# Kernel optimization log

Hardware: AMD Instinct MI355X
Metric: run time of the kernel (lower is better)

## Reference

```python
import math
import jax, jax.numpy as jnp
import numpy as np

DIM = 1536
HEADS = 8
DK = 64
DV = 192
NRPF = 192  # num_rel_pos_features, divisible by 6
SEQ = 1536
BATCH = 4
SCALE = DK ** -0.5


def get_positional_embed(n, feature_size):
    # distances in [-(n-1), n-1], length 2n-1
    dist = jnp.arange(-n + 1, n).astype(jnp.float32)
    adist = jnp.abs(dist)[:, None]  # [2n-1, 1]
    f = feature_size // 6  # 3 feature fns, each doubled by sign channel
    # exponential half-life features
    max_range = math.log(n) / math.log(2.0)
    half_life = 2.0 ** jnp.linspace(3.0, max_range, f)[None, :]
    emb_exp = jnp.exp(-math.log(2.0) / half_life * adist)
    # central mask features
    center_widths = (2.0 ** jnp.arange(1, f + 1).astype(jnp.float32) - 1.0)[None, :]
    emb_cm = (center_widths > adist).astype(jnp.float32)
    # gamma pdf features
    stddev = n / (2.0 * f)
    start_mean = n / float(f)
    mean = jnp.linspace(start_mean, float(n), f)[None, :]
    conc = (mean / stddev) ** 2
    rate = mean / stddev ** 2
    log_unnorm = (conc - 1.0) * jnp.log(jnp.maximum(adist, 1e-20)) - rate * adist
    log_norm = jax.scipy.special.gammaln(conc) - conc * jnp.log(rate)
    prob = jnp.exp(log_unnorm - log_norm) + 1e-8
    emb_g = prob / jnp.max(prob, axis=-1, keepdims=True)
    emb = jnp.concatenate([emb_exp, emb_cm, emb_g], axis=-1)  # [2n-1, feat/2]
    return jnp.concatenate([emb, jnp.sign(dist)[:, None] * emb], axis=-1)  # [2n-1, feat]


def relative_shift(x):
    # x: [b, h, n, 2n-1] -> [b, h, n, n] via the Transformer-XL shift trick
    b, h, t1, t2 = x.shape
    x = jnp.concatenate([jnp.zeros_like(x[..., :1]), x], axis=-1)  # [b,h,t1,t2+1]
    x = x.reshape(b, h, t2 + 1, t1)[:, :, 1:, :].reshape(b, h, t1, t2)
    return x[..., : (t2 + 2) // 2]


def layer_norm(x, g, b, eps=1e-5):
    mu = jnp.mean(x, axis=-1, keepdims=True)
    var = jnp.var(x, axis=-1, keepdims=True)
    return (x - mu) * jax.lax.rsqrt(var + eps) * g + b


def setup_inputs() -> dict:
    key = jax.random.key(0)
    ks = jax.random.split(key, 16)
    d, h, dk, dv = DIM, HEADS, DK, DV
    inp = {
        "x": jax.random.normal(ks[0], (BATCH, SEQ, d), dtype=jnp.float32),
        "ln1_g": jnp.ones((d,), jnp.float32),
        "ln1_b": jnp.zeros((d,), jnp.float32),
        "Wq": jax.random.normal(ks[1], (d, h * dk), jnp.float32) / math.sqrt(d),
        "Wk": jax.random.normal(ks[2], (d, h * dk), jnp.float32) / math.sqrt(d),
        "Wv": jax.random.normal(ks[3], (d, h * dv), jnp.float32) / math.sqrt(d),
        "Wo": jax.random.normal(ks[4], (h * dv, d), jnp.float32) / math.sqrt(h * dv),
        "bo": jnp.zeros((d,), jnp.float32),
        "Wrk": jax.random.normal(ks[5], (NRPF, h * dk), jnp.float32) / math.sqrt(NRPF),
        "rel_content_bias": jax.random.normal(ks[6], (1, h, 1, dk), jnp.float32),
        "rel_pos_bias": jax.random.normal(ks[7], (1, h, 1, dk), jnp.float32),
        "ln2_g": jnp.ones((d,), jnp.float32),
        "ln2_b": jnp.zeros((d,), jnp.float32),
        "W1": jax.random.normal(ks[8], (d, 2 * d), jnp.float32) / math.sqrt(d),
        "b1": jnp.zeros((2 * d,), jnp.float32),
        "W2": jax.random.normal(ks[9], (2 * d, d), jnp.float32) / math.sqrt(2 * d),
        "b2": jnp.zeros((d,), jnp.float32),
    }
    return inp


def _attention(x, Wq, Wk, Wv, Wo, bo, Wrk, rel_content_bias, rel_pos_bias):
    b, n, _ = x.shape
    h, dk, dv = HEADS, DK, DV
    q = (x @ Wq).reshape(b, n, h, dk).transpose(0, 2, 1, 3) * SCALE  # [b,h,n,dk]
    k = (x @ Wk).reshape(b, n, h, dk).transpose(0, 2, 1, 3)
    v = (x @ Wv).reshape(b, n, h, dv).transpose(0, 2, 1, 3)
    content_logits = jnp.einsum('bhid,bhjd->bhij', q + rel_content_bias, k)
    positions = get_positional_embed(n, NRPF)  # [2n-1, NRPF]
    rel_k = (positions @ Wrk).reshape(2 * n - 1, h, dk).transpose(1, 0, 2)  # [h,2n-1,dk]
    rel_logits = jnp.einsum('bhid,hjd->bhij', q + rel_pos_bias, rel_k)
    rel_logits = relative_shift(rel_logits)  # [b,h,n,n]
    attn = jax.nn.softmax(content_logits + rel_logits, axis=-1)
    out = jnp.einsum('bhij,bhjd->bhid', attn, v)
    out = out.transpose(0, 2, 1, 3).reshape(b, n, h * dv)
    return out @ Wo + bo


def reference(x, ln1_g, ln1_b, Wq, Wk, Wv, Wo, bo, Wrk, rel_content_bias,
              rel_pos_bias, ln2_g, ln2_b, W1, b1, W2, b2):
    # pre-LN attention with residual
    x = x + _attention(layer_norm(x, ln1_g, ln1_b), Wq, Wk, Wv, Wo, bo, Wrk,
                       rel_content_bias, rel_pos_bias)
    # MLP block (carries its own LayerNorm and residual)
    y = layer_norm(x, ln2_g, ln2_b)
    y = jax.nn.relu(y @ W1 + b1)
    y = y @ W2 + b2
    return y + x
```

## Files before the change

### kernel.cpp

```cpp
#include <hip/hip_runtime.h>
#include <hip/hip_bf16.h>
#include <math.h>

#define SEQN 1536
#define NH 8
#define MROWS 6144
#define NDIST 3071

typedef __attribute__((ext_vector_type(8))) _Float16 f16x8;
typedef __attribute__((ext_vector_type(4))) _Float16 f16x4;
typedef __attribute__((ext_vector_type(4))) float f32x4;

#define MFMAH(a, b, c) __builtin_amdgcn_mfma_f32_16x16x32_f16(a, b, c, 0, 0, 0)

__device__ __forceinline__ void gl_lds16(const void* g, void* l) {
  __builtin_amdgcn_global_load_lds(
      (const __attribute__((address_space(1))) void*)g,
      (__attribute__((address_space(3))) void*)l, 16, 0, 0);
}

__global__ __launch_bounds__(64) void pos_embed_kernel(float* __restrict__ pos) {
  int row = blockIdx.x;
  int j = threadIdx.x;
  if (j >= 32) return;
  float dist = (float)(row - (SEQN - 1));
  float adist = fabsf(dist);
  float sgn = (dist > 0.f) ? 1.f : (dist < 0.f ? -1.f : 0.f);

  const float max_range = 10.58496250072116f;
  float hl = exp2f(3.0f + ((max_range - 3.0f) / 31.0f) * (float)j);
  float e_exp = expf(-0.6931471805599453f / hl * adist);

  float cw = exp2f((float)(j + 1)) - 1.0f;
  float e_cm = (cw > adist) ? 1.0f : 0.0f;

  float mean = 48.0f * (float)(j + 1);
  float tt = mean / 24.0f;
  float conc = tt * tt;
  float rate = mean / 576.0f;
  float log_unnorm = (conc - 1.0f) * logf(fmaxf(adist, 1e-20f)) - rate * adist;
  float log_norm = lgammaf(conc) - conc * logf(rate);
  float prob = expf(log_unnorm - log_norm) + 1e-8f;
  float mx = prob;
  #pragma unroll
  for (int off = 16; off >= 1; off >>= 1)
    mx = fmaxf(mx, __shfl_xor(mx, off, 32));
  float e_g = prob / mx;

  float* o = pos + (size_t)row * 192;
  o[j] = e_exp;        o[32 + j] = e_cm;        o[64 + j] = e_g;
  o[96 + j] = sgn * e_exp; o[128 + j] = sgn * e_cm; o[160 + j] = sgn * e_g;
}

__global__ __launch_bounds__(512) void relk_kernel(
    const float* __restrict__ pos, const float* __restrict__ Wrk,
    const float* __restrict__ pb, _Float16* __restrict__ rk, float* __restrict__ PR) {
  __shared__ float prow[16][192];
  const int d0 = blockIdx.x * 16;
  const int t = threadIdx.x;
  #pragma unroll
  for (int p = 0; p < 6; ++p) {
    int idx = t + p * 512;
    int r = idx / 192, c = idx - r * 192;
    prow[r][c] = pos[(size_t)(d0 + r) * 192 + c];
  }
  __syncthreads();
  float acc[16];
  #pragma unroll
  for (int r = 0; r < 16; ++r) acc[r] = 0.f;
  #pragma unroll 4
  for (int kk = 0; kk < 192; ++kk) {
    float wv = Wrk[(size_t)kk * 512 + t];
    #pragma unroll
    for (int r = 0; r < 16; ++r) acc[r] = fmaf(prow[r][kk], wv, acc[r]);
  }
  #pragma unroll
  for (int r = 0; r < 16; ++r)
    rk[(size_t)(d0 + r) * 512 + t] = (_Float16)acc[r];
  float pbv = pb[t];
  #pragma unroll
  for (int r = 0; r < 16; ++r) {
    float pv = pbv * acc[r];
    #pragma unroll
    for (int off = 32; off >= 1; off >>= 1) pv += __shfl_xor(pv, off);
    if ((t & 63) == 0 && (d0 + r) < NDIST)
      PR[(size_t)(t >> 6) * NDIST + d0 + r] = pv;
  }
}

__global__ __launch_bounds__(256) void ck_kernel(
    const _Float16* __restrict__ Kp, const float* __restrict__ cb,
    float* __restrict__ CK) {
  const int gid = blockIdx.x * 4 + (threadIdx.x >> 6);
  const int lane = threadIdx.x & 63;
  const int row = gid >> 3;
  const int h = gid & 7;
  float kv = (float)Kp[(size_t)row * 512 + h * 64 + lane];
  float pv = cb[h * 64 + lane] * kv;
  #pragma unroll
  for (int off = 32; off >= 1; off >>= 1) pv += __shfl_xor(pv, off);
  if (lane == 0) CK[(size_t)row * 8 + h] = pv;
}

__global__ __launch_bounds__(256) void ln_kernel(
    const float* __restrict__ x, const float* __restrict__ g,
    const float* __restrict__ bta, _Float16* __restrict__ oh) {
  const int row = blockIdx.x;
  const int t = threadIdx.x;
  __shared__ float red[4];
  __shared__ float bc[2];
  const float4* xr = (const float4*)(x + (size_t)row * 1536);
  float4 v0 = xr[t];
  float4 v1 = make_float4(0.f, 0.f, 0.f, 0.f);
  if (t < 128) v1 = xr[256 + t];
  float s = v0.x + v0.y + v0.z + v0.w;
  if (t < 128) s += v1.x + v1.y + v1.z + v1.w;
  #pragma unroll
  for (int off = 32; off >= 1; off >>= 1) s += __shfl_xor(s, off);
  if ((t & 63) == 0) red[t >> 6] = s;
  __syncthreads();
  if (t == 0) bc[0] = (red[0] + red[1] + red[2] + red[3]) * (1.f / 1536.f);
  __syncthreads();
  const float mu = bc[0];
  float d, s2 = 0.f;
  d = v0.x - mu; s2 += d * d; d = v0.y - mu; s2 += d * d;
  d = v0.z - mu; s2 += d * d; d = v0.w - mu; s2 += d * d;
  if (t < 128) {
    d = v1.x - mu; s2 += d * d; d = v1.y - mu; s2 += d * d;
    d = v1.z - mu; s2 += d * d; d = v1.w - mu; s2 += d * d;
  }
  #pragma unroll
  for (int off = 32; off >= 1; off >>= 1) s2 += __shfl_xor(s2, off);
  if ((t & 63) == 0) red[t >> 6] = s2;
  __syncthreads();
  if (t == 0) bc[1] = (red[0] + red[1] + red[2] + red[3]) * (1.f / 1536.f);
  __syncthreads();
  const float inv = rsqrtf(bc[1] + 1e-5f);
  const float4* g4 = (const float4*)g;
  const float4* b4 = (const float4*)bta;
  float4 gg = g4[t], bb = b4[t];
  f16x4 hv;
  hv[0] = (_Float16)((v0.x - mu) * inv * gg.x + bb.x);
  hv[1] = (_Float16)((v0.y - mu) * inv * gg.y + bb.y);
  hv[2] = (_Float16)((v0.z - mu) * inv * gg.z + bb.z);
  hv[3] = (_Float16)((v0.w - mu) * inv * gg.w + bb.w);
  *(f16x4*)(oh + (size_t)row * 1536 + t * 4) = hv;
  if (t < 128) {
    gg = g4[256 + t]; bb = b4[256 + t];
    hv[0] = (_Float16)((v1.x - mu) * inv * gg.x + bb.x);
    hv[1] = (_Float16)((v1.y - mu) * inv * gg.y + bb.y);
    hv[2] = (_Float16)((v1.z - mu) * inv * gg.z + bb.z);
    hv[3] = (_Float16)((v1.w - mu) * inv * gg.w + bb.w);
    *(f16x4*)(oh + (size_t)row * 1536 + 1024 + t * 4) = hv;
  }
}

__global__ __launch_bounds__(256) void convw_kernel(
    const float* __restrict__ W, _Float16* __restrict__ Th,
    int N, int K, int KD, int roff, float scale) {
  __shared__ float tile[32][33];
  const int n0 = blockIdx.x * 32, k0 = blockIdx.y * 32;
  const int t = threadIdx.x;
  const int cr = t >> 5;
  const int cc = t & 31;
  #pragma unroll
  for (int p = 0; p < 4; ++p) {
    int r = cr + p * 8;
    tile[r][cc] = W[(size_t)(k0 + r) * N + n0 + cc];
  }
  __syncthreads();
  #pragma unroll
  for (int p = 0; p < 4; ++p) {
    int r = cr + p * 8;
    float v = tile[cc][r] * scale;
    Th[(size_t)(roff + n0 + r) * KD + k0 + cc] = (_Float16)v;
  }
}

template <int EPI, int BNJ>
__global__ __launch_bounds__(256, 4) void mgemm_kernel(
    const _Float16* __restrict__ A, const _Float16* __restrict__ B,
    float* __restrict__ C, _Float16* __restrict__ Ch,
    _Float16* __restrict__ Kp, _Float16* __restrict__ Vt,
    const float* __restrict__ bias, const float* __restrict__ res,
    int M, int N, int K) {
  constexpr int BN = BNJ * 32;
  __shared__ _Float16 sm[8192 + BN * 64];
  const int t = threadIdx.x;
  const int lane = t & 63;
  const int w = t >> 6;
  const int wm = w >> 1, wn = w & 1;
  const int slab = (M >> 7) >> 3;
  const int xcd = blockIdx.x & 7;
  const int r = blockIdx.x >> 3;
  const int yt = xcd * slab + (r % slab);
  const int xt = r / slab;
  const int m0 = yt * 128, n0 = xt * BN;

  f32x4 acc[4][BNJ];
  #pragma unroll
  for (int i = 0; i < 4; ++i)
    #pragma unroll
    for (int j = 0; j < BNJ; ++j) acc[i][j] = (f32x4){0.f, 0.f, 0.f, 0.f};

  const int srow = t >> 3;
  const int ssl = t & 7;
  const int ss = ssl ^ (srow & 7);
  const int lr = lane & 15;
  const int g = lane >> 4;
  const int kb = lr & 7;

  for (int k0 = 0; k0 < K; k0 += 64) {
    #pragma unroll
    for (int p = 0; p < 4; ++p) {
      int row = srow + p * 32;
      gl_lds16(A + (size_t)(m0 + row) * K + k0 + ss * 8, &sm[row * 64 + ssl * 8]);
    }
    #pragma unroll
    for (int p = 0; p < BN / 32; ++p) {
      int row = srow + p * 32;
      gl_lds16(B + (size_t)(n0 + row) * K + k0 + ss * 8,
               &sm[8192 + row * 64 + ssl * 8]);
    }
    __syncthreads();
    #pragma unroll
    for (int h2 = 0; h2 < 2; ++h2) {
      const int ksl = ((h2 * 4 + g) ^ kb) * 8;
      f16x8 a[4], b[BNJ];
      #pragma unroll
      for (int i = 0; i < 4; ++i)
        a[i] = *(const f16x8*)(&sm[(wm * 64 + i * 16 + lr) * 64 + ksl]);
      #pragma unroll
      for (int j = 0; j < BNJ; ++j)
        b[j] = *(const f16x8*)(&sm[8192 + (wn * BNJ * 16 + j * 16 + lr) * 64 + ksl]);
      #pragma unroll
      for (int i = 0; i < 4; ++i)
        #pragma unroll
        for (int j = 0; j < BNJ; ++j)
          acc[i][j] = MFMAH(a[i], b[j], acc[i][j]);
    }
    __syncthreads();
  }

  const int lq = lane >> 4;
  #pragma unroll
  for (int i = 0; i < 4; ++i) {
    #pragma unroll
    for (int j = 0; j < BNJ; ++j) {
      const int c0 = n0 + wn * BNJ * 16 + j * 16;
      const int col = c0 + lr;
      const int rbase = m0 + wm * 64 + i * 16 + lq * 4;
      if (EPI == 3) {
        #pragma unroll
        for (int q = 0; q < 4; ++q) {
          size_t o = (size_t)(rbase + q) * N + col;
          C[o] = acc[i][j][q] + bias[col] + res[o];
        }
      } else if (EPI == 2) {
        #pragma unroll
        for (int q = 0; q < 4; ++q) {
          size_t o = (size_t)(rbase + q) * N + col;
          Ch[o] = (_Float16)fmaxf(acc[i][j][q] + bias[col], 0.f);
        }
      } else {
        if (c0 < 512) {
          #pragma unroll
          for (int q = 0; q < 4; ++q)
            Ch[(size_t)(rbase + q) * 512 + col] = (_Float16)acc[i][j][q];
        } else if (c0 < 1024) {
          #pragma unroll
          for (int q = 0; q < 4; ++q)
            Kp[(size_t)(rbase + q) * 512 + (col - 512)] = (_Float16)acc[i][j][q];
        } else {
          int dv = col - 1024;
          int hd = dv / 192;
          int dvh = dv - hd * 192;
          int bb = rbase / 1536;
          int nloc = rbase - bb * 1536;
          f16x4 pk;
          pk[0] = (_Float16)acc[i][j][0];
          pk[1] = (_Float16)acc[i][j][1];
          pk[2] = (_Float16)acc[i][j][2];
          pk[3] = (_Float16)acc[i][j][3];
          *(f16x4*)(Vt + (((size_t)bb * 8 + hd) * 192 + dvh) * 1536 + nloc) = pk;
        }
      }
    }
  }
}

__global__ __launch_bounds__(256, 3) void attn_kernel(
    const _Float16* __restrict__ Qp, const _Float16* __restrict__ Kp,
    const _Float16* __restrict__ Vt, const _Float16* __restrict__ rk,
    const float* __restrict__ PR, const float* __restrict__ CK,
    _Float16* __restrict__ ao) {
  __shared__ _Float16 lds[26752];
  const int id = blockIdx.x;
  const int xcd = id & 7, s = id >> 3;
  const int bh = xcd * 4 + s / 24;
  const int it = s % 24;
  const int b = bh >> 3, h = bh & 7;
  const int t = threadIdx.x;
  const int w = t >> 6;
  const int lane = t & 63;
  const int c15 = lane & 15, g = lane >> 4;
  const int swz = c15 & 7;
  const int vsz = (c15 >> 1) & 3;
  const int qrow0 = it * 64 + w * 16;
  const int rrow0 = 48 - w * 16;
  const int R0 = 1472 - it * 64;

  const int lr = lane >> 3, sl = lane & 7;
  const int ss = sl ^ lr;
  const int ss2 = (lane & 3) ^ ((lane >> 3) & 3);

  f16x8 qh0, qh1;
  {
    size_t qo = ((size_t)(b * SEQN + qrow0 + c15)) * 512 + h * 64 + g * 8;
    qh0 = *(const f16x8*)(Qp + qo);
    qh1 = *(const f16x8*)(Qp + qo + 32);
  }
  const float* PRrow = PR + (size_t)h * NDIST;
  const float* CKb2 = CK + (size_t)b * SEQN * 8 + h;

  f32x4 acc[12];
  #pragma unroll
  for (int d = 0; d < 12; ++d) acc[d] = (f32x4){0.f, 0.f, 0.f, 0.f};
  float mrun[4], lrun[4];
  #pragma unroll
  for (int q = 0; q < 4; ++q) { mrun[q] = -1e30f; lrun[q] = 0.f; }

  #define STAGE_KV(J0, KB, VB)                                                   \
    do {                                                                         \
      size_t gk = ((size_t)(b * SEQN + (J0) + w * 8 + lr)) * 512 + h * 64 + ss * 8; \
      gl_lds16(Kp + gk, &lds[(KB) + w * 512]);                                   \
      _Pragma("unroll") for (int p = 0; p < 3; ++p) {                            \
        int rv = w * 48 + p * 16 + (lane >> 2);                                  \
        size_t gv = (((size_t)(b * 8 + h)) * 192 + rv) * SEQN + (J0) + ss2 * 8;  \
        gl_lds16(Vt + gv, &lds[(VB) + (w * 48 + p * 16) * 32]);                  \
      }                                                                          \
    } while (0)

  #define STAGE_R_PRO()                                                          \
    do {                                                                         \
      _Pragma("unroll") for (int p = 0; p < 4; ++p) {                            \
        int rr = w * 32 + p * 8 + lr;                                            \
        size_t gr = ((size_t)(R0 + rr)) * 512 + h * 64 + ss * 8;                 \
        gl_lds16(rk + gr, &lds[16384 + (w * 32 + p * 8) * 64]);                  \
      }                                                                          \
    } while (0)

  #define STAGE_R_INC(REL0)                                                      \
    do {                                                                         \
      int rr = (REL0) + w * 8 + lr;                                              \
      size_t gr = ((size_t)(R0 + rr)) * 512 + h * 64 + ss * 8;                   \
      gl_lds16(rk + gr, &lds[16384 + ((((REL0) + w * 8) & 127)) * 64]);          \
    } while (0)

  #define COMP_T(DST, ETOFF)                                                     \
    do {                                                                         \
      int relrow = (cc32 + rrow0 + (ETOFF) + c15) & 127;                         \
      f16x8 r0_ = *(const f16x8*)(&lds[16384 + relrow * 64 + (g ^ swz) * 8]);    \
      f16x8 r1_ = *(const f16x8*)(&lds[16384 + relrow * 64 + ((4 + g) ^ swz) * 8]); \
      f32x4 tt_ = (f32x4){0.f, 0.f, 0.f, 0.f};                                   \
      tt_ = MFMAH(qh0, r0_, tt_);                                                \
      tt_ = MFMAH(qh1, r1_, tt_);                                                \
      float prv_ = PRrow[dbase + (ETOFF) + c15];                                 \
      _Pragma("unroll") for (int q = 0; q < 4; ++q) tt_[q] += prv_;              \
      DST = tt_;                                                                 \
    } while (0)

  STAGE_KV(0, 0, 4096);
  STAGE_R_PRO();

  f32x4 T0, T1, T2;

  for (int c = 0; c < 48; ++c) {
    const int j0 = c * 32;
    const int cc32 = c * 32;
    const int cur = c & 1;
    const int KB = cur * 2048;
    const int VB = 4096 + cur * 6144;
    __syncthreads();

    if (c < 47) STAGE_KV(j0 + 32, (cur ^ 1) * 2048, 4096 + (cur ^ 1) * 6144);

    const int dbase = 1520 + j0 - qrow0;
    __builtin_amdgcn_s_setprio(1);
    if (c == 0) {
      COMP_T(T0, 0);
    } else {
      T0 = T2;
    }
    COMP_T(T1, 16);
    COMP_T(T2, 32);
    f32x4 S[2];
    #pragma unroll
    for (int st = 0; st < 2; ++st) {
      int rowK = st * 16 + c15;
      f16x8 kh0 = *(const f16x8*)(&lds[KB + rowK * 64 + (g ^ swz) * 8]);
      f16x8 kh1 = *(const f16x8*)(&lds[KB + rowK * 64 + ((4 + g) ^ swz) * 8]);
      f32x4 ssv = (f32x4){0.f, 0.f, 0.f, 0.f};
      ssv = MFMAH(qh0, kh0, ssv);
      ssv = MFMAH(qh1, kh1, ssv);
      S[st] = ssv;
    }
    __builtin_amdgcn_s_setprio(0);
    float ck0 = CKb2[(size_t)(j0 + c15) * 8];
    float ck1 = CKb2[(size_t)(j0 + 16 + c15) * 8];
    #pragma unroll
    for (int q = 0; q < 4; ++q) {
      int eoff = c15 + 15 - 4 * g - q;
      int src = (lane & 48) | (eoff & 15);
      float t0v = __shfl(T0[q], src);
      float t1v = __shfl(T1[q], src);
      float t2v = __shfl(T2[q], src);
      bool lo = eoff < 16;
      S[0][q] += ck0 + (lo ? t0v : t1v);
      S[1][q] += ck1 + (lo ? t1v : t2v);
    }
    int need = 0;
    #pragma unroll
    for (int st = 0; st < 2; ++st)
      #pragma unroll
      for (int q = 0; q < 4; ++q) need |= (S[st][q] > mrun[q] + 8.0f) ? 1 : 0;
    if (__any(need)) {
      float mx[4];
      #pragma unroll
      for (int q = 0; q < 4; ++q) mx[q] = fmaxf(S[0][q], S[1][q]);
      #pragma unroll
      for (int off = 8; off >= 1; off >>= 1)
        #pragma unroll
        for (int q = 0; q < 4; ++q) mx[q] = fmaxf(mx[q], __shfl_xor(mx[q], off));
      #pragma unroll
      for (int q = 0; q < 4; ++q) {
        float mn = fmaxf(mrun[q], mx[q]);
        float al = __expf(mrun[q] - mn);
        mrun[q] = mn;
        lrun[q] *= al;
        #pragma unroll
        for (int d = 0; d < 12; ++d) acc[d][q] *= al;
      }
    }
    float pv16[2][4], sum[4];
    #pragma unroll
    for (int q = 0; q < 4; ++q) sum[q] = 0.f;
    #pragma unroll
    for (int st = 0; st < 2; ++st)
      #pragma unroll
      for (int q = 0; q < 4; ++q) {
        float p = __expf(S[st][q] - mrun[q]);
        sum[q] += p;
        pv16[st][q] = p;
      }
    #pragma unroll
    for (int off = 8; off >= 1; off >>= 1)
      #pragma unroll
      for (int q = 0; q < 4; ++q) sum[q] += __shfl_xor(sum[q], off);
    #pragma unroll
    for (int q = 0; q < 4; ++q) lrun[q] += sum[q];

    #pragma unroll
    for (int st = 0; st < 2; ++st)
      #pragma unroll
      for (int q = 0; q < 4; ++q)
        lds[24576 + (w * 16 + 4 * g + q) * 34 + st * 16 + c15] = (_Float16)pv16[st][q];

    __syncthreads();

    if (c >= 1 && c < 47) STAGE_R_INC(cc32 + 96);

    f16x8 pf = *(const f16x8*)(&lds[24576 + (w * 16 + c15) * 34 + g * 8]);
    __builtin_amdgcn_s_setprio(1);
    #pragma unroll
    for (int d = 0; d < 12; ++d) {
      int rowV = d * 16 + c15;
      f16x8 vf = *(const f16x8*)(&lds[VB + rowV * 32 + (g ^ vsz) * 8]);
      acc[d] = MFMAH(pf, vf, acc[d]);
    }
    __builtin_amdgcn_s_setprio(0);
  }

  float rinv[4];
  #pragma unroll
  for (int q = 0; q < 4; ++q) rinv[q] = 1.0f / lrun[q];
  #pragma unroll
  for (int d = 0; d < 12; ++d) {
    int col = h * 192 + d * 16 + c15;
    #pragma unroll
    for (int q = 0; q < 4; ++q) {
      size_t row = (size_t)(b * SEQN + qrow0 + 4 * g + q);
      ao[row * 1536 + col] = (_Float16)(acc[d][q] * rinv[q]);
    }
  }
  #undef STAGE_KV
  #undef STAGE_R_PRO
  #undef STAGE_R_INC
  #undef COMP_T
}

extern "C" void kernel_launch(void* const* d_in, const int* in_sizes, int n_in,
                              void* d_out, int out_size, void* d_ws, size_t ws_size,
                              hipStream_t stream) {
  (void)in_sizes; (void)n_in; (void)out_size; (void)ws_size;
  const float* x   = (const float*)d_in[0];
  const float* g1  = (const float*)d_in[1];
  const float* be1 = (const float*)d_in[2];
  const float* Wq  = (const float*)d_in[3];
  const float* Wk  = (const float*)d_in[4];
  const float* Wv  = (const float*)d_in[5];
  const float* Wo  = (const float*)d_in[6];
  const float* bo  = (const float*)d_in[7];
  const float* Wrk = (const float*)d_in[8];
  const float* cb  = (const float*)d_in[9];
  const float* pb  = (const float*)d_in[10];
  const float* g2  = (const float*)d_in[11];
  const float* be2 = (const float*)d_in[12];
  const float* W1  = (const float*)d_in[13];
  const float* b1  = (const float*)d_in[14];
  const float* W2  = (const float*)d_in[15];
  const float* b2  = (const float*)d_in[16];
  float* out = (float*)d_out;

  char* B = (char*)d_ws;
  float* pos     = (float*)(B + 0);
  _Float16* rk   = (_Float16*)(B + 2359296);
  float* PRb     = (float*)(B + 5505024);
  float* CKb     = (float*)(B + 5603328);
  _Float16* xn   = (_Float16*)(B + 5799936);
  _Float16* Wb   = (_Float16*)(B + 24674304);
  _Float16* Qp   = (_Float16*)(B + 34111488);
  _Float16* Kp   = (_Float16*)(B + 40402944);
  _Float16* Vtp  = (_Float16*)(B + 46694400);
  _Float16* ao   = (_Float16*)(B + 65568768);
  float* x2      = (float*)(B + 84443136);
  _Float16* h1   = (_Float16*)(B + 122191872);

  pos_embed_kernel<<<NDIST, 64, 0, stream>>>(pos);
  relk_kernel<<<192, 512, 0, stream>>>(pos, Wrk, pb, rk, PRb);
  ln_kernel<<<MROWS, 256, 0, stream>>>(x, g1, be1, xn);
  convw_kernel<<<dim3(16, 48), 256, 0, stream>>>(Wq, Wb, 512, 1536, 1536, 0, 0.125f);
  convw_kernel<<<dim3(16, 48), 256, 0, stream>>>(Wk, Wb, 512, 1536, 1536, 512, 1.0f);
  convw_kernel<<<dim3(48, 48), 256, 0, stream>>>(Wv, Wb, 1536, 1536, 1536, 1024, 1.0f);
  mgemm_kernel<4, 4><<<960, 256, 0, stream>>>(
      xn, Wb, nullptr, Qp, Kp, Vtp, nullptr, nullptr, MROWS, 2560, 1536);
  ck_kernel<<<MROWS * 2, 256, 0, stream>>>(Kp, cb, CKb);
  attn_kernel<<<768, 256, 0, stream>>>(Qp, Kp, Vtp, rk, PRb, CKb, ao);
  convw_kernel<<<dim3(48, 48), 256, 0, stream>>>(Wo, Wb, 1536, 1536, 1536, 0, 1.0f);
  mgemm_kernel<3, 3><<<768, 256, 0, stream>>>(
      ao, Wb, x2, nullptr, nullptr, nullptr, bo, x, MROWS, 1536, 1536);
  ln_kernel<<<MROWS, 256, 0, stream>>>(x2, g2, be2, xn);
  convw_kernel<<<dim3(96, 48), 256, 0, stream>>>(W1, Wb, 3072, 1536, 1536, 0, 1.0f);
  mgemm_kernel<2, 4><<<1152, 256, 0, stream>>>(
      xn, Wb, nullptr, h1, nullptr, nullptr, b1, nullptr, MROWS, 3072, 1536);
  convw_kernel<<<dim3(48, 96), 256, 0, stream>>>(W2, Wb, 1536, 3072, 3072, 0, 1.0f);
  mgemm_kernel<3, 3><<<768, 256, 0, stream>>>(
      h1, Wb, out, nullptr, nullptr, nullptr, b2, x2, MROWS, 1536, 3072);
}
```

Baseline: 463.0 us.

## Compute softmax denominator via MFMA and drop per-iteration barrier in attention

The attention loop now gets the softmax row sum from an extra MFMA against a ones vector, replacing the shuffle-based reduction and the lrun bookkeeping. The second __syncthreads per iteration is removed because each wave only reads the P tile it wrote itself, and the rel-k prefetch moves up to sit next to the K/V prefetch. The FFN1 GEMM switches to a wider N tile (BN=192) with fewer blocks and a launch bound of 3 per SM. The trade-off is one extra MFMA per iteration, more accumulator registers, and fp16-rounded P values feeding the denominator.

```diff
diff --git a/kernel.cpp b/kernel.cpp
--- a/kernel.cpp
+++ b/kernel.cpp
@@ -177,8 +177,8 @@
   }
 }
 
-template <int EPI, int BNJ>
-__global__ __launch_bounds__(256, 4) void mgemm_kernel(
+template <int EPI, int BNJ, int MW>
+__global__ __launch_bounds__(256, MW) void mgemm_kernel(
     const _Float16* __restrict__ A, const _Float16* __restrict__ B,
     float* __restrict__ C, _Float16* __restrict__ Ch,
     _Float16* __restrict__ Kp, _Float16* __restrict__ Vt,
@@ -320,15 +320,18 @@
     qh0 = *(const f16x8*)(Qp + qo);
     qh1 = *(const f16x8*)(Qp + qo + 32);
   }
+  f16x8 ones;
+  #pragma unroll
+  for (int i = 0; i < 8; ++i) ones[i] = (_Float16)1.0f;
   const float* PRrow = PR + (size_t)h * NDIST;
   const float* CKb2 = CK + (size_t)b * SEQN * 8 + h;
 
-  f32x4 acc[12];
-  #pragma unroll
-  for (int d = 0; d < 12; ++d) acc[d] = (f32x4){0.f, 0.f, 0.f, 0.f};
-  float mrun[4], lrun[4];
-  #pragma unroll
-  for (int q = 0; q < 4; ++q) { mrun[q] = -1e30f; lrun[q] = 0.f; }
+  f32x4 acc[13];
+  #pragma unroll
+  for (int d = 0; d < 13; ++d) acc[d] = (f32x4){0.f, 0.f, 0.f, 0.f};
+  float mrun[4];
+  #pragma unroll
+  for (int q = 0; q < 4; ++q) mrun[q] = -1e30f;
 
   #define STAGE_KV(J0, KB, VB)                                                   \
     do {                                                                         \
@@ -383,7 +386,10 @@
     const int VB = 4096 + cur * 6144;
     __syncthreads();
 
-    if (c < 47) STAGE_KV(j0 + 32, (cur ^ 1) * 2048, 4096 + (cur ^ 1) * 6144);
+    if (c < 47) {
+      STAGE_KV(j0 + 32, (cur ^ 1) * 2048, 4096 + (cur ^ 1) * 6144);
+      if (c >= 1) STAGE_R_INC(cc32 + 96);
+    }
 
     const int dbase = 1520 + j0 - qrow0;
     __builtin_amdgcn_s_setprio(1);
@@ -437,38 +443,16 @@
         float mn = fmaxf(mrun[q], mx[q]);
         float al = __expf(mrun[q] - mn);
         mrun[q] = mn;
-        lrun[q] *= al;
         #pragma unroll
-        for (int d = 0; d < 12; ++d) acc[d][q] *= al;
+        for (int d = 0; d < 13; ++d) acc[d][q] *= al;
       }
     }
-    float pv16[2][4], sum[4];
-    #pragma unroll
-    for (int q = 0; q < 4; ++q) sum[q] = 0.f;
     #pragma unroll
     for (int st = 0; st < 2; ++st)
       #pragma unroll
-      for (int q = 0; q < 4; ++q) {
-        float p = __expf(S[st][q] - mrun[q]);
-        sum[q] += p;
-        pv16[st][q] = p;
-      }
-    #pragma unroll
-    for (int off = 8; off >= 1; off >>= 1)
-      #pragma unroll
-      for (int q = 0; q < 4; ++q) sum[q] += __shfl_xor(sum[q], off);
-    #pragma unroll
-    for (int q = 0; q < 4; ++q) lrun[q] += sum[q];
-
-    #pragma unroll
-    for (int st = 0; st < 2; ++st)
-      #pragma unroll
       for (int q = 0; q < 4; ++q)
-        lds[24576 + (w * 16 + 4 * g + q) * 34 + st * 16 + c15] = (_Float16)pv16[st][q];
-
-    __syncthreads();
-
-    if (c >= 1 && c < 47) STAGE_R_INC(cc32 + 96);
+        lds[24576 + (w * 16 + 4 * g + q) * 34 + st * 16 + c15] =
+            (_Float16)__expf(S[st][q] - mrun[q]);
 
     f16x8 pf = *(const f16x8*)(&lds[24576 + (w * 16 + c15) * 34 + g * 8]);
     __builtin_amdgcn_s_setprio(1);
@@ -478,12 +462,13 @@
       f16x8 vf = *(const f16x8*)(&lds[VB + rowV * 32 + (g ^ vsz) * 8]);
       acc[d] = MFMAH(pf, vf, acc[d]);
     }
+    acc[12] = MFMAH(pf, ones, acc[12]);
     __builtin_amdgcn_s_setprio(0);
   }
 
   float rinv[4];
   #pragma unroll
-  for (int q = 0; q < 4; ++q) rinv[q] = 1.0f / lrun[q];
+  for (int q = 0; q < 4; ++q) rinv[q] = 1.0f / acc[12][q];
   #pragma unroll
   for (int d = 0; d < 12; ++d) {
     int col = h * 192 + d * 16 + c15;
@@ -542,18 +527,18 @@
   convw_kernel<<<dim3(16, 48), 256, 0, stream>>>(Wq, Wb, 512, 1536, 1536, 0, 0.125f);
   convw_kernel<<<dim3(16, 48), 256, 0, stream>>>(Wk, Wb, 512, 1536, 1536, 512, 1.0f);
   convw_kernel<<<dim3(48, 48), 256, 0, stream>>>(Wv, Wb, 1536, 1536, 1536, 1024, 1.0f);
-  mgemm_kernel<4, 4><<<960, 256, 0, stream>>>(
+  mgemm_kernel<4, 4, 4><<<960, 256, 0, stream>>>(
       xn, Wb, nullptr, Qp, Kp, Vtp, nullptr, nullptr, MROWS, 2560, 1536);
   ck_kernel<<<MROWS * 2, 256, 0, stream>>>(Kp, cb, CKb);
   attn_kernel<<<768, 256, 0, stream>>>(Qp, Kp, Vtp, rk, PRb, CKb, ao);
   convw_kernel<<<dim3(48, 48), 256, 0, stream>>>(Wo, Wb, 1536, 1536, 1536, 0, 1.0f);
-  mgemm_kernel<3, 3><<<768, 256, 0, stream>>>(
+  mgemm_kernel<3, 3, 4><<<768, 256, 0, stream>>>(
       ao, Wb, x2, nullptr, nullptr, nullptr, bo, x, MROWS, 1536, 1536);
   ln_kernel<<<MROWS, 256, 0, stream>>>(x2, g2, be2, xn);
   convw_kernel<<<dim3(96, 48), 256, 0, stream>>>(W1, Wb, 3072, 1536, 1536, 0, 1.0f);
-  mgemm_kernel<2, 4><<<1152, 256, 0, stream>>>(
+  mgemm_kernel<2, 6, 3><<<768, 256, 0, stream>>>(
       xn, Wb, nullptr, h1, nullptr, nullptr, b1, nullptr, MROWS, 3072, 1536);
   convw_kernel<<<dim3(48, 96), 256, 0, stream>>>(W2, Wb, 1536, 3072, 3072, 0, 1.0f);
-  mgemm_kernel<3, 3><<<768, 256, 0, stream>>>(
+  mgemm_kernel<3, 3, 4><<<768, 256, 0, stream>>>(
       h1, Wb, out, nullptr, nullptr, nullptr, b2, x2, MROWS, 1536, 3072);
 }
```

Measured after the change: 427.1 us. -7.8%, faster.
